# Performance work log

Hardware: AMD Instinct MI355X
Metric: run time of the kernel (lower is better)

The kernel has to match this reference:

```python
import jax, jax.numpy as jnp
import numpy as np

N_NODES = 100000
N_EDGES = 1250000
D_IN, D_HID, D_OUT = 64, 32, 41


def setup_inputs() -> dict:
    key = jax.random.key(0)
    ks = jax.random.split(key, 7)
    x = jax.random.normal(ks[0], (N_NODES, D_IN), dtype=jnp.float32)
    edge_index = jax.random.randint(ks[1], (2, N_EDGES), 0, N_NODES, dtype=jnp.int64)
    # PyG SAGEConv params: lin_l (applied to aggregated neighbors, has bias),
    # lin_r (applied to root, no bias). Stored here as [in, out] matrices.
    W1l = jax.random.normal(ks[2], (D_IN, D_HID), dtype=jnp.float32) / np.sqrt(D_IN)
    b1 = jnp.zeros((D_HID,), dtype=jnp.float32)
    W1r = jax.random.normal(ks[3], (D_IN, D_HID), dtype=jnp.float32) / np.sqrt(D_IN)
    W2l = jax.random.normal(ks[4], (D_HID, D_OUT), dtype=jnp.float32) / np.sqrt(D_HID)
    b2 = jnp.zeros((D_OUT,), dtype=jnp.float32)
    W2r = jax.random.normal(ks[5], (D_HID, D_OUT), dtype=jnp.float32) / np.sqrt(D_HID)
    return {"x": x, "edge_index": edge_index, "W1l": W1l, "b1": b1, "W1r": W1r,
            "W2l": W2l, "b2": b2, "W2r": W2r}


def _sage_conv(h, src, dst, n_nodes, Wl, b, Wr):
    # mean-aggregate source features at destination nodes (PyG default aggr='mean')
    msg = h[src]  # [E, d] irregular gather
    agg = jax.ops.segment_sum(msg, dst, num_segments=n_nodes)
    cnt = jax.ops.segment_sum(jnp.ones((src.shape[0],), dtype=h.dtype), dst,
                              num_segments=n_nodes)
    agg = agg / jnp.maximum(cnt, 1.0)[:, None]
    return agg @ Wl + b + h @ Wr


def reference(x, edge_index, W1l, b1, W1r, W2l, b2, W2r):
    src, dst = edge_index[0], edge_index[1]
    n = x.shape[0]
    h = _sage_conv(x, src, dst, n, W1l, b1, W1r)
    h = jax.nn.relu(h)
    # F.dropout(training=self.training) -> identity in eval/inference mode
    out = _sage_conv(h, src, dst, n, W2l, b2, W2r)
    return out
```

## Files before the change

### kernel.cpp

```cpp
#include <hip/hip_runtime.h>

#define N_NODES 100000
#define N_EDGES 1250000
#define D_IN 64
#define D_HID 32
#define D_OUT 41
#define NBUK 784
#define BSH 7
#define PARTB 256
#define BCHUNK 4883
#define SCAP 32
#define BSTR 8192
#define PBLK 782
#define ROWCAP 48
#define LSTR 88
#define OSTR 72
#define ZERO_OFF 6400000
#define SENT 0x01000000u

typedef short bf16x8 __attribute__((ext_vector_type(8)));
typedef float f32x4 __attribute__((ext_vector_type(4)));

__device__ __forceinline__ float bflo(unsigned int u) {
    union { unsigned int i; float f; } v; v.i = u << 16; return v.f;
}
__device__ __forceinline__ float bfhi(unsigned int u) {
    union { unsigned int i; float f; } v; v.i = u & 0xffff0000u; return v.f;
}
__device__ __forceinline__ unsigned short f2bf(float f) {
    union { float f; unsigned int i; } v; v.f = f;
    unsigned int x = v.i;
    return (unsigned short)((x + 0x7fffu + ((x >> 16) & 1u)) >> 16);
}
__device__ __forceinline__ void acc8(float* a, uint4 u) {
    a[0] += bflo(u.x); a[1] += bfhi(u.x);
    a[2] += bflo(u.y); a[3] += bfhi(u.y);
    a[4] += bflo(u.z); a[5] += bfhi(u.z);
    a[6] += bflo(u.w); a[7] += bfhi(u.w);
}
__device__ __forceinline__ int padded8(int d) {
    int dd = d < ROWCAP ? d : ROWCAP;
    int p = (dd + 7) & ~7;
    if (p == 0) p = 8;
    return p;
}

__device__ __forceinline__ void chunk8(const int* row, int i, const char* tab,
                                       int qb, float* a) {
    int4 o0 = *(const int4*)(row + i);
    int4 o1 = *(const int4*)(row + i + 4);
    uint4 u0 = *(const uint4*)(tab + o0.x + qb);
    uint4 u1 = *(const uint4*)(tab + o0.y + qb);
    uint4 u2 = *(const uint4*)(tab + o0.z + qb);
    uint4 u3 = *(const uint4*)(tab + o0.w + qb);
    uint4 u4 = *(const uint4*)(tab + o1.x + qb);
    uint4 u5 = *(const uint4*)(tab + o1.y + qb);
    uint4 u6 = *(const uint4*)(tab + o1.z + qb);
    uint4 u7 = *(const uint4*)(tab + o1.w + qb);
    acc8(a, u0); acc8(a, u1); acc8(a, u2); acc8(a, u3);
    acc8(a, u4); acc8(a, u5); acc8(a, u6); acc8(a, u7);
}

__device__ __forceinline__ void insh(unsigned int w, int lo, int* lists, int* lcnt) {
    if (w < SENT) {
        int dl = (int)(w >> 17) - lo;
        if ((unsigned)dl < 64u) {
            int p = atomicAdd(&lcnt[dl], 1);
            if (p < ROWCAP) lists[dl * ROWCAP + p] = (int)((w & 0x1FFFFu) << 6);
        }
    }
}

__global__ __launch_bounds__(256) void k_front(const int* __restrict__ src,
                                               const int* __restrict__ dst,
                                               unsigned int* __restrict__ buckets,
                                               const float* __restrict__ x,
                                               const float* __restrict__ W1l,
                                               const float* __restrict__ W1r,
                                               const float* __restrict__ b1,
                                               unsigned short* __restrict__ xl,
                                               unsigned short* __restrict__ xr) {
    __shared__ short smem[128 * LSTR + 64 * LSTR];
    int tid = threadIdx.x;
    if (blockIdx.x < PARTB) {
        int* lcnt = (int*)smem;
        int bid = blockIdx.x;
        for (int i = tid; i < NBUK; i += 256) lcnt[i] = 0;
        __syncthreads();
        int e0 = bid * BCHUNK;
        int e1 = e0 + BCHUNK; if (e1 > N_EDGES) e1 = N_EDGES;
        int e = e0 + tid;
        for (; e + 768 < e1; e += 1024) {
            int d0 = dst[e],       s0 = src[e];
            int d1 = dst[e + 256], s1 = src[e + 256];
            int d2 = dst[e + 512], s2 = src[e + 512];
            int d3 = dst[e + 768], s3 = src[e + 768];
            int b0 = d0 >> BSH, p0 = atomicAdd(&lcnt[b0], 1);
            if (p0 < SCAP) buckets[(size_t)b0 * BSTR + bid * SCAP + p0] =
                (unsigned int)s0 | ((unsigned int)(d0 & 127) << 17);
            int b1i = d1 >> BSH, p1 = atomicAdd(&lcnt[b1i], 1);
            if (p1 < SCAP) buckets[(size_t)b1i * BSTR + bid * SCAP + p1] =
                (unsigned int)s1 | ((unsigned int)(d1 & 127) << 17);
            int b2 = d2 >> BSH, p2 = atomicAdd(&lcnt[b2], 1);
            if (p2 < SCAP) buckets[(size_t)b2 * BSTR + bid * SCAP + p2] =
                (unsigned int)s2 | ((unsigned int)(d2 & 127) << 17);
            int b3 = d3 >> BSH, p3 = atomicAdd(&lcnt[b3], 1);
            if (p3 < SCAP) buckets[(size_t)b3 * BSTR + bid * SCAP + p3] =
                (unsigned int)s3 | ((unsigned int)(d3 & 127) << 17);
        }
        for (; e < e1; e += 256) {
            int d = dst[e], s = src[e];
            int b = d >> BSH;
            int p = atomicAdd(&lcnt[b], 1);
            if (p < SCAP) buckets[(size_t)b * BSTR + bid * SCAP + p] =
                (unsigned int)s | ((unsigned int)(d & 127) << 17);
        }
        return;
    }
    short* sX  = smem;
    short* sWT = smem + 128 * LSTR;
    int n0 = (blockIdx.x - PARTB) * 128;
    for (int i = tid; i < 1024; i += 256) {
        int k = i >> 4, c4 = i & 15;
        float4 v = (c4 < 8) ? ((const float4*)W1l)[k * 8 + c4]
                            : ((const float4*)W1r)[k * 8 + (c4 - 8)];
        int col = c4 * 4;
        sWT[(col + 0) * LSTR + k] = (short)f2bf(v.x);
        sWT[(col + 1) * LSTR + k] = (short)f2bf(v.y);
        sWT[(col + 2) * LSTR + k] = (short)f2bf(v.z);
        sWT[(col + 3) * LSTR + k] = (short)f2bf(v.w);
    }
    {
        int g = tid >> 1, q2 = tid & 1;
        int n = n0 + g;
        short pk[32];
        if (n < N_NODES) {
            const float4* xp = (const float4*)(x + (size_t)n * D_IN + q2 * 32);
#pragma unroll
            for (int i = 0; i < 8; ++i) {
                float4 f = xp[i];
                pk[i * 4 + 0] = (short)f2bf(f.x);
                pk[i * 4 + 1] = (short)f2bf(f.y);
                pk[i * 4 + 2] = (short)f2bf(f.z);
                pk[i * 4 + 3] = (short)f2bf(f.w);
            }
        } else {
#pragma unroll
            for (int i = 0; i < 32; ++i) pk[i] = 0;
        }
        short* sp = sX + g * LSTR + q2 * 32;
        *(bf16x8*)(sp)      = *(bf16x8*)(pk);
        *(bf16x8*)(sp + 8)  = *(bf16x8*)(pk + 8);
        *(bf16x8*)(sp + 16) = *(bf16x8*)(pk + 16);
        *(bf16x8*)(sp + 24) = *(bf16x8*)(pk + 24);
    }
    __syncthreads();
    int wid = tid >> 6, lane = tid & 63;
    int quad = lane >> 4, lc = lane & 15;
    const short* saA = sX + (wid * 16 + lc) * LSTR + quad * 8;
    const short* saB = sX + ((wid + 4) * 16 + lc) * LSTR + quad * 8;
    bf16x8 afA0 = *(const bf16x8*)(saA);
    bf16x8 afA1 = *(const bf16x8*)(saA + 32);
    bf16x8 afB0 = *(const bf16x8*)(saB);
    bf16x8 afB1 = *(const bf16x8*)(saB + 32);
    __syncthreads();
    short* sO = sX;
#pragma unroll
    for (int mm = 0; mm < 2; ++mm) {
        int m0 = (wid + mm * 4) * 16;
        bf16x8 af0 = mm ? afB0 : afA0;
        bf16x8 af1 = mm ? afB1 : afA1;
#pragma unroll
        for (int t = 0; t < 4; ++t) {
            const short* sbp = sWT + (t * 16 + lc) * LSTR + quad * 8;
            bf16x8 bf0 = *(const bf16x8*)(sbp);
            bf16x8 bf1 = *(const bf16x8*)(sbp + 32);
            f32x4 acc = {0.f, 0.f, 0.f, 0.f};
            acc = __builtin_amdgcn_mfma_f32_16x16x32_bf16(af0, bf0, acc, 0, 0, 0);
            acc = __builtin_amdgcn_mfma_f32_16x16x32_bf16(af1, bf1, acc, 0, 0, 0);
            int col = t * 16 + lc;
            float bias = (col >= 32) ? b1[col - 32] : 0.f;
#pragma unroll
            for (int r = 0; r < 4; ++r)
                sO[(m0 + (quad << 2) + r) * OSTR + col] = (short)f2bf(acc[r] + bias);
        }
    }
    __syncthreads();
    {
        int g = tid >> 1, q2 = tid & 1;
        int n = n0 + g;
        const short* srow = sO + g * OSTR + q2 * 32;
        uint4 v0, v1, v2, v3;
        if (n < N_NODES) {
            v0 = *(const uint4*)(srow);
            v1 = *(const uint4*)(srow + 8);
            v2 = *(const uint4*)(srow + 16);
            v3 = *(const uint4*)(srow + 24);
        } else {
            v0 = v1 = v2 = v3 = make_uint4(0, 0, 0, 0);
        }
        char* base = (char*)(q2 ? xr : xl) + ((size_t)n << 6);
        *(uint4*)(base)      = v0;
        *(uint4*)(base + 16) = v1;
        *(uint4*)(base + 32) = v2;
        *(uint4*)(base + 48) = v3;
    }
}

__global__ __launch_bounds__(256) void k_bagg1(const unsigned int* __restrict__ bukspace,
                                               const unsigned short* __restrict__ xl,
                                               const unsigned short* __restrict__ xr,
                                               unsigned short* __restrict__ h,
                                               int* __restrict__ glists,
                                               int* __restrict__ gcnt) {
    __shared__ int lists[64 * ROWCAP];
    __shared__ int lcnt[64];
    int tid = threadIdx.x;
    int buk = blockIdx.x >> 1, half = blockIdx.x & 1;
    int lo = half << 6;
    if (tid < 64) lcnt[tid] = 0;
    __syncthreads();
    const uint4* bk4 = (const uint4*)(bukspace + (size_t)buk * BSTR);
#pragma unroll
    for (int k = 0; k < BSTR / 4 / 256; ++k) {
        uint4 w = bk4[tid + k * 256];
        insh(w.x, lo, lists, lcnt);
        insh(w.y, lo, lists, lcnt);
        insh(w.z, lo, lists, lcnt);
        insh(w.w, lo, lists, lcnt);
    }
    __syncthreads();
    if (tid < 64) {
        int c = lcnt[tid];
        int cc = c < ROWCAP ? c : ROWCAP;
        int ce = (cc + 7) & ~7;
        if (ce == 0) ce = 8;
        for (int s = cc; s < ce; ++s) lists[tid * ROWCAP + s] = ZERO_OFF;
    }
    __syncthreads();
    int nbase = (buk << BSH) + lo;
    for (int i4 = tid; i4 < 64 * 12; i4 += 256) {
        int li = i4 / 12, c4 = i4 % 12;
        if (c4 * 4 < padded8(lcnt[li]))
            *(uint4*)(glists + (size_t)(nbase + li) * ROWCAP + c4 * 4) =
                *(const uint4*)(lists + li * ROWCAP + c4 * 4);
    }
    if (tid < 64) gcnt[nbase + tid] = lcnt[tid];
    int g = tid >> 2, q = tid & 3, qb = q << 4;
    int n = nbase + g;
    int d = lcnt[g];
    int p = padded8(d);
    const int* row = lists + g * ROWCAP;
    const char* xlb = (const char*)xl;
    float a[8] = {0.f, 0.f, 0.f, 0.f, 0.f, 0.f, 0.f, 0.f};
    chunk8(row, 0, xlb, qb, a);
    for (int i = 8; i < p; i += 8) chunk8(row, i, xlb, qb, a);
    if (n >= N_NODES) {
        *(uint4*)((char*)h + ((size_t)n << 6) + qb) = make_uint4(0, 0, 0, 0);
        return;
    }
    float inv = 1.0f / fmaxf((float)d, 1.0f);
    uint4 rr = *(const uint4*)((const char*)xr + ((size_t)n << 6) + qb);
    float o0 = fmaxf(a[0] * inv + bflo(rr.x), 0.f);
    float o1 = fmaxf(a[1] * inv + bfhi(rr.x), 0.f);
    float o2 = fmaxf(a[2] * inv + bflo(rr.y), 0.f);
    float o3 = fmaxf(a[3] * inv + bfhi(rr.y), 0.f);
    float o4 = fmaxf(a[4] * inv + bflo(rr.z), 0.f);
    float o5 = fmaxf(a[5] * inv + bfhi(rr.z), 0.f);
    float o6 = fmaxf(a[6] * inv + bflo(rr.w), 0.f);
    float o7 = fmaxf(a[7] * inv + bfhi(rr.w), 0.f);
    uint4 o;
    o.x = ((unsigned int)f2bf(o1) << 16) | f2bf(o0);
    o.y = ((unsigned int)f2bf(o3) << 16) | f2bf(o2);
    o.z = ((unsigned int)f2bf(o5) << 16) | f2bf(o4);
    o.w = ((unsigned int)f2bf(o7) << 16) | f2bf(o6);
    *(uint4*)((char*)h + ((size_t)n << 6) + qb) = o;
}

__global__ __launch_bounds__(256) void k_bagg2(const int* __restrict__ glists,
                                               const int* __restrict__ gcnt,
                                               const unsigned short* __restrict__ h,
                                               const float* __restrict__ W2l,
                                               const float* __restrict__ b2,
                                               const float* __restrict__ W2r,
                                               float* __restrict__ out) {
    __shared__ short sBT[48 * LSTR];
    __shared__ short sA[64 * LSTR];
    int tid = threadIdx.x;
    int buk = blockIdx.x >> 1, half = blockIdx.x & 1;
    int nbase = (buk << BSH) + (half << 6);
    for (int i = tid; i < 48 * 64; i += 256) {
        int col = i >> 6, kk = i & 63;
        float v = 0.f;
        if (col < D_OUT) v = (kk < 32) ? W2l[kk * D_OUT + col] : W2r[(kk - 32) * D_OUT + col];
        sBT[col * LSTR + kk] = (short)f2bf(v);
    }
    int g = tid >> 2, q = tid & 3, qb = q << 4;
    int n = nbase + g;
    bool ok = (n < N_NODES);
    int d = gcnt[n];
    int p = padded8(d);
    const int* row = glists + (size_t)n * ROWCAP;
    const char* hb = (const char*)h;
    float a[8] = {0.f, 0.f, 0.f, 0.f, 0.f, 0.f, 0.f, 0.f};
    chunk8(row, 0, hb, qb, a);
    for (int i = 8; i < p; i += 8) chunk8(row, i, hb, qb, a);
    {
        float inv = 1.0f / fmaxf((float)d, 1.0f);
        short pk[8];
#pragma unroll
        for (int j = 0; j < 8; ++j) pk[j] = (short)f2bf(a[j] * inv);
        uint4 hr = ok ? *(const uint4*)(hb + ((size_t)n << 6) + qb)
                      : make_uint4(0, 0, 0, 0);
        short* sp = sA + g * LSTR + q * 8;
        *(bf16x8*)(sp)     = *(bf16x8*)pk;
        *(uint4*)(sp + 32) = hr;
    }
    __syncthreads();
    int wid = tid >> 6, lane = tid & 63;
    int quad = lane >> 4, lc = lane & 15;
    const short* sa = sA + (wid * 16 + lc) * LSTR + quad * 8;
    bf16x8 af0 = *(const bf16x8*)(sa);
    bf16x8 af1 = *(const bf16x8*)(sa + 32);
#pragma unroll
    for (int t = 0; t < 3; ++t) {
        const short* sbp = sBT + (t * 16 + lc) * LSTR + quad * 8;
        bf16x8 bf0 = *(const bf16x8*)(sbp);
        bf16x8 bf1 = *(const bf16x8*)(sbp + 32);
        f32x4 acc = {0.f, 0.f, 0.f, 0.f};
        acc = __builtin_amdgcn_mfma_f32_16x16x32_bf16(af0, bf0, acc, 0, 0, 0);
        acc = __builtin_amdgcn_mfma_f32_16x16x32_bf16(af1, bf1, acc, 0, 0, 0);
        int j = t * 16 + lc;
        if (j < D_OUT) {
            float bias = b2[j];
#pragma unroll
            for (int r = 0; r < 4; ++r) {
                int n2 = nbase + wid * 16 + (quad << 2) + r;
                if (n2 < N_NODES) out[(size_t)n2 * D_OUT + j] = acc[r] + bias;
            }
        }
    }
}

extern "C" void kernel_launch(void* const* d_in, const int* in_sizes, int n_in,
                              void* d_out, int out_size, void* d_ws, size_t ws_size,
                              hipStream_t stream) {
    const float* x   = (const float*)d_in[0];
    const int*   ei  = (const int*)d_in[1];
    const int*   src = ei;
    const int*   dst = ei + N_EDGES;
    const float* W1l = (const float*)d_in[2];
    const float* b1  = (const float*)d_in[3];
    const float* W1r = (const float*)d_in[4];
    const float* W2l = (const float*)d_in[5];
    const float* b2  = (const float*)d_in[6];
    const float* W2r = (const float*)d_in[7];
    float* out = (float*)d_out;

    int* iws = (int*)d_ws;
    unsigned int* bukspace = (unsigned int*)iws;
    int* glists = iws + 6422528;
    int* gcnt   = iws + 11239424;
    unsigned short* xl = (unsigned short*)(iws + 11339776);
    unsigned short* xr = (unsigned short*)(iws + 12945408);
    unsigned short* h  = (unsigned short*)(iws + 14551040);

    k_front<<<PARTB + PBLK, 256, 0, stream>>>(src, dst, bukspace,
                                              x, W1l, W1r, b1, xl, xr);
    k_bagg1<<<2 * NBUK, 256, 0, stream>>>(bukspace, xl, xr, h, glists, gcnt);
    k_bagg2<<<2 * NBUK, 256, 0, stream>>>(glists, gcnt, h, W2l, b2, W2r, out);
}
```

Baseline: 165.8 us.

## Process each bucket with one 512-thread block and store lists in place

```diff
diff --git a/kernel.cpp b/kernel.cpp
--- a/kernel.cpp
+++ b/kernel.cpp
@@ -61,13 +61,11 @@
     acc8(a, u4); acc8(a, u5); acc8(a, u6); acc8(a, u7);
 }
 
-__device__ __forceinline__ void insh(unsigned int w, int lo, int* lists, int* lcnt) {
+__device__ __forceinline__ void ins(unsigned int w, int* lists, int* lcnt) {
     if (w < SENT) {
-        int dl = (int)(w >> 17) - lo;
-        if ((unsigned)dl < 64u) {
-            int p = atomicAdd(&lcnt[dl], 1);
-            if (p < ROWCAP) lists[dl * ROWCAP + p] = (int)((w & 0x1FFFFu) << 6);
-        }
+        int dl = (int)(w >> 17);
+        int p = atomicAdd(&lcnt[dl], 1);
+        if (p < ROWCAP) lists[dl * ROWCAP + p] = (int)((w & 0x1FFFFu) << 6);
     }
 }
 
@@ -207,30 +205,27 @@
     }
 }
 
-__global__ __launch_bounds__(256) void k_bagg1(const unsigned int* __restrict__ bukspace,
+__global__ __launch_bounds__(512) void k_bagg1(unsigned int* __restrict__ bukspace,
                                                const unsigned short* __restrict__ xl,
                                                const unsigned short* __restrict__ xr,
                                                unsigned short* __restrict__ h,
-                                               int* __restrict__ glists,
                                                int* __restrict__ gcnt) {
-    __shared__ int lists[64 * ROWCAP];
-    __shared__ int lcnt[64];
-    int tid = threadIdx.x;
-    int buk = blockIdx.x >> 1, half = blockIdx.x & 1;
-    int lo = half << 6;
-    if (tid < 64) lcnt[tid] = 0;
-    __syncthreads();
-    const uint4* bk4 = (const uint4*)(bukspace + (size_t)buk * BSTR);
-#pragma unroll
-    for (int k = 0; k < BSTR / 4 / 256; ++k) {
-        uint4 w = bk4[tid + k * 256];
-        insh(w.x, lo, lists, lcnt);
-        insh(w.y, lo, lists, lcnt);
-        insh(w.z, lo, lists, lcnt);
-        insh(w.w, lo, lists, lcnt);
-    }
-    __syncthreads();
-    if (tid < 64) {
+    __shared__ int lists[128 * ROWCAP];
+    __shared__ int lcnt[128];
+    int tid = threadIdx.x, b = blockIdx.x;
+    if (tid < 128) lcnt[tid] = 0;
+    __syncthreads();
+    const uint4* bk4 = (const uint4*)(bukspace + (size_t)b * BSTR);
+#pragma unroll
+    for (int k = 0; k < BSTR / 4 / 512; ++k) {
+        uint4 w = bk4[tid + k * 512];
+        ins(w.x, lists, lcnt);
+        ins(w.y, lists, lcnt);
+        ins(w.z, lists, lcnt);
+        ins(w.w, lists, lcnt);
+    }
+    __syncthreads();
+    if (tid < 128) {
         int c = lcnt[tid];
         int cc = c < ROWCAP ? c : ROWCAP;
         int ce = (cc + 7) & ~7;
@@ -238,14 +233,15 @@
         for (int s = cc; s < ce; ++s) lists[tid * ROWCAP + s] = ZERO_OFF;
     }
     __syncthreads();
-    int nbase = (buk << BSH) + lo;
-    for (int i4 = tid; i4 < 64 * 12; i4 += 256) {
+    int nbase = b << BSH;
+    int* glists = (int*)(bukspace + (size_t)b * BSTR);
+    for (int i4 = tid; i4 < 128 * 12; i4 += 512) {
         int li = i4 / 12, c4 = i4 % 12;
         if (c4 * 4 < padded8(lcnt[li]))
-            *(uint4*)(glists + (size_t)(nbase + li) * ROWCAP + c4 * 4) =
+            *(uint4*)(glists + li * ROWCAP + c4 * 4) =
                 *(const uint4*)(lists + li * ROWCAP + c4 * 4);
     }
-    if (tid < 64) gcnt[nbase + tid] = lcnt[tid];
+    if (tid < 128) gcnt[nbase + tid] = lcnt[tid];
     int g = tid >> 2, q = tid & 3, qb = q << 4;
     int n = nbase + g;
     int d = lcnt[g];
@@ -277,7 +273,7 @@
     *(uint4*)((char*)h + ((size_t)n << 6) + qb) = o;
 }
 
-__global__ __launch_bounds__(256) void k_bagg2(const int* __restrict__ glists,
+__global__ __launch_bounds__(512) void k_bagg2(const unsigned int* __restrict__ bukspace,
                                                const int* __restrict__ gcnt,
                                                const unsigned short* __restrict__ h,
                                                const float* __restrict__ W2l,
@@ -285,22 +281,22 @@
                                                const float* __restrict__ W2r,
                                                float* __restrict__ out) {
     __shared__ short sBT[48 * LSTR];
-    __shared__ short sA[64 * LSTR];
-    int tid = threadIdx.x;
-    int buk = blockIdx.x >> 1, half = blockIdx.x & 1;
-    int nbase = (buk << BSH) + (half << 6);
-    for (int i = tid; i < 48 * 64; i += 256) {
+    __shared__ short sA[128 * LSTR];
+    int tid = threadIdx.x, b = blockIdx.x;
+    int nbase = b << BSH;
+    for (int i = tid; i < 48 * 64; i += 512) {
         int col = i >> 6, kk = i & 63;
         float v = 0.f;
         if (col < D_OUT) v = (kk < 32) ? W2l[kk * D_OUT + col] : W2r[(kk - 32) * D_OUT + col];
         sBT[col * LSTR + kk] = (short)f2bf(v);
     }
+    const int* glists = (const int*)(bukspace + (size_t)b * BSTR);
     int g = tid >> 2, q = tid & 3, qb = q << 4;
     int n = nbase + g;
     bool ok = (n < N_NODES);
     int d = gcnt[n];
     int p = padded8(d);
-    const int* row = glists + (size_t)n * ROWCAP;
+    const int* row = glists + g * ROWCAP;
     const char* hb = (const char*)h;
     float a[8] = {0.f, 0.f, 0.f, 0.f, 0.f, 0.f, 0.f, 0.f};
     chunk8(row, 0, hb, qb, a);
@@ -359,14 +355,13 @@
 
     int* iws = (int*)d_ws;
     unsigned int* bukspace = (unsigned int*)iws;
-    int* glists = iws + 6422528;
-    int* gcnt   = iws + 11239424;
-    unsigned short* xl = (unsigned short*)(iws + 11339776);
-    unsigned short* xr = (unsigned short*)(iws + 12945408);
-    unsigned short* h  = (unsigned short*)(iws + 14551040);
+    int* gcnt   = iws + 6422528;
+    unsigned short* xl = (unsigned short*)(iws + 6522880);
+    unsigned short* xr = (unsigned short*)(iws + 8128512);
+    unsigned short* h  = (unsigned short*)(iws + 9734144);
 
     k_front<<<PARTB + PBLK, 256, 0, stream>>>(src, dst, bukspace,
                                               x, W1l, W1r, b1, xl, xr);
-    k_bagg1<<<2 * NBUK, 256, 0, stream>>>(bukspace, xl, xr, h, glists, gcnt);
-    k_bagg2<<<2 * NBUK, 256, 0, stream>>>(glists, gcnt, h, W2l, b2, W2r, out);
-}
+    k_bagg1<<<NBUK, 512, 0, stream>>>(bukspace, xl, xr, h, gcnt);
+    k_bagg2<<<NBUK, 512, 0, stream>>>(bukspace, gcnt, h, W2l, b2, W2r, out);
+}
```

Result: no change. 162.9 us (-1.8%).
